# Kernel optimization log

Hardware: AMD Instinct MI355X
Metric: run time of the kernel (lower is better)

Reference implementation:

```python
import jax, jax.numpy as jnp
import numpy as np


def setup_inputs() -> dict:
    key = jax.random.key(0)
    k1, k2, k3 = jax.random.split(key, 3)
    N_GRAPHS, NUM_NODES, DEGREES = 4, 100000, 128
    BATCH = 50000
    adj_ins = jax.random.randint(k1, (N_GRAPHS, NUM_NODES, DEGREES), 0, NUM_NODES, dtype=jnp.int32)
    adj_outs = jax.random.randint(k2, (N_GRAPHS, NUM_NODES, DEGREES), 0, NUM_NODES, dtype=jnp.int32)
    ids = jax.random.randint(k3, (BATCH,), 0, NUM_NODES, dtype=jnp.int32)
    return {
        "adj_ins": adj_ins,
        "adj_outs": adj_outs,
        "g_id": 1,
        "ids": ids,
        "num_samples": 32,
        "ins": 1,
    }


def reference(adj_ins, adj_outs, g_id, ids, num_samples, ins):
    # tf.random_shuffle on the transposed [degrees, batch] matrix applies ONE
    # random permutation to the column (neighbor) axis, shared across all rows.
    adj = adj_ins if ins else adj_outs                 # [G, N, D]
    degrees = adj.shape[2]
    cur_adj_info = adj[g_id]                            # [N, D]  (slice + reshape)
    adj_lists = cur_adj_info[ids]                       # [B, D]  gather (embedding_lookup)
    perm = jax.random.permutation(jax.random.key(42), degrees)
    sel = perm[:num_samples]                            # first num_samples of shuffled cols
    return jnp.take(adj_lists, sel, axis=1)             # [B, num_samples]
```

## Files before the change

kernel.cpp:

```cpp
#include <hip/hip_runtime.h>
#include <algorithm>


static inline void tf2x32_host(unsigned k0, unsigned k1, unsigned c0, unsigned c1,
                               unsigned& o0, unsigned& o1) {
  const unsigned ks0 = k0, ks1 = k1, ks2 = k0 ^ k1 ^ 0x1BD11BDAu;
  unsigned x0 = c0 + ks0, x1 = c1 + ks1;
#define TF_R(r) { x0 += x1; x1 = (x1 << (r)) | (x1 >> (32 - (r))); x1 ^= x0; }
  TF_R(13) TF_R(15) TF_R(26) TF_R(6)   x0 += ks1; x1 += ks2 + 1u;
  TF_R(17) TF_R(29) TF_R(16) TF_R(24)  x0 += ks2; x1 += ks0 + 2u;
  TF_R(13) TF_R(15) TF_R(26) TF_R(6)   x0 += ks0; x1 += ks1 + 3u;
  TF_R(17) TF_R(29) TF_R(16) TF_R(24)  x0 += ks1; x1 += ks2 + 4u;
  TF_R(13) TF_R(15) TF_R(26) TF_R(6)   x0 += ks2; x1 += ks0 + 5u;
#undef TF_R
  o0 = x0; o1 = x1;
}

#define MAX_NS 64
struct SelArgs { int v[MAX_NS]; };

#define ROWS_PB 8
#define DEG_MAX 128
__global__ __launch_bounds__(256) void gather_rows_kernel(
    const int* __restrict__ adj_ins, const int* __restrict__ adj_outs,
    const int* __restrict__ g_id_p, const int* __restrict__ ids,
    const int* __restrict__ ins_p, const SelArgs sel,
    int batch, int ns, int num_nodes, int degrees,
    int* __restrict__ out) {
  __shared__ int s_row[ROWS_PB][DEG_MAX];
  __shared__ int s_sel[MAX_NS];

  const int t = threadIdx.x;
  const int r0 = blockIdx.x * ROWS_PB;

  if (t < ns) s_sel[t] = sel.v[t];

  const int* adj = (*ins_p) ? adj_ins : adj_outs;
  const long long base = (long long)(*g_id_p) * (long long)num_nodes * (long long)degrees;

  {
    const int row = t >> 5;
    const int lane = t & 31;
    const int r = r0 + row;
    if (r < batch) {
      const int node = ids[r];
      const int* rp = adj + base + (long long)node * degrees;
      for (int c = lane * 4; c < degrees; c += 32 * 4) {
        const int4 v = *(const int4*)(rp + c);
        *(int4*)&s_row[row][c] = v;
      }
    }
  }
  __syncthreads();

  for (int e = t; e < ROWS_PB * ns; e += 256) {
    const int row = e / ns;
    const int j = e - row * ns;
    const int r = r0 + row;
    if (r < batch) out[(long long)r * ns + j] = s_row[row][s_sel[j]];
  }
}

extern "C" void kernel_launch(void* const* d_in, const int* in_sizes, int n_in,
                              void* d_out, int out_size, void* d_ws, size_t ws_size,
                              hipStream_t stream) {
  const int* adj_ins  = (const int*)d_in[0];
  const int* adj_outs = (const int*)d_in[1];
  const int* g_id_p   = (const int*)d_in[2];
  const int* ids      = (const int*)d_in[3];
  const int* ins_p    = (const int*)d_in[5];

  const int batch = in_sizes[3];
  const int ns    = out_size / batch;
  const int NUM_NODES = 100000;
  const int DEGREES   = 128;

  unsigned sk0, sk1;
  tf2x32_host(0u, 42u, 0u, 1u, sk0, sk1);
  unsigned bits[DEG_MAX];
  int perm[DEG_MAX];
  for (int i = 0; i < DEGREES; ++i) {
    unsigned b1, b2;
    tf2x32_host(sk0, sk1, 0u, (unsigned)i, b1, b2);
    bits[i] = b1 ^ b2;
    perm[i] = i;
  }
  std::stable_sort(perm, perm + DEGREES,
                   [&](int a, int b) { return bits[a] < bits[b]; });
  SelArgs sel{};
  const int ns_c = ns > MAX_NS ? MAX_NS : ns;
  for (int j = 0; j < ns_c; ++j) sel.v[j] = perm[j];

  const int nblocks = (batch + ROWS_PB - 1) / ROWS_PB;
  gather_rows_kernel<<<nblocks, 256, 0, stream>>>(
      adj_ins, adj_outs, g_id_p, ids, ins_p, sel,
      batch, ns, NUM_NODES, DEGREES, (int*)d_out);
}
```

Measured before the change: 323.0 us.

## Replace shared-memory row staging with direct per-element gather of selected columns

Drops the staging of full adjacency rows in shared memory and the block barrier. Each thread now computes one output element and loads only the selected column straight from global memory. The aim is to avoid fetching unused columns and to remove the synchronisation, in exchange for uncoalesced scattered 4-byte loads within each row.

Result: no change. 322.7 us (-0.1%).

```diff
diff --git a/kernel.cpp b/kernel.cpp
--- a/kernel.cpp
+++ b/kernel.cpp
@@ -17,48 +17,33 @@
 }
 
 #define MAX_NS 64
+
 struct SelArgs { int v[MAX_NS]; };
 
-#define ROWS_PB 8
-#define DEG_MAX 128
-__global__ __launch_bounds__(256) void gather_rows_kernel(
+__global__ __launch_bounds__(256) void gather_direct_kernel(
     const int* __restrict__ adj_ins, const int* __restrict__ adj_outs,
     const int* __restrict__ g_id_p, const int* __restrict__ ids,
     const int* __restrict__ ins_p, const SelArgs sel,
     int batch, int ns, int num_nodes, int degrees,
     int* __restrict__ out) {
-  __shared__ int s_row[ROWS_PB][DEG_MAX];
-  __shared__ int s_sel[MAX_NS];
+  const long long gid = (long long)blockIdx.x * 256 + threadIdx.x;
 
-  const int t = threadIdx.x;
-  const int r0 = blockIdx.x * ROWS_PB;
-
-  if (t < ns) s_sel[t] = sel.v[t];
+  int r, j;
+  if (ns == 32) {
+    r = (int)(gid >> 5);
+    j = (int)(gid & 31);
+  } else {
+    r = (int)(gid / ns);
+    j = (int)(gid - (long long)r * (long long)ns);
+  }
+  if (r >= batch) return;
 
   const int* adj = (*ins_p) ? adj_ins : adj_outs;
-  const long long base = (long long)(*g_id_p) * (long long)num_nodes * (long long)degrees;
+  const long long base =
+      (long long)(*g_id_p) * (long long)num_nodes * (long long)degrees;
 
-  {
-    const int row = t >> 5;
-    const int lane = t & 31;
-    const int r = r0 + row;
-    if (r < batch) {
-      const int node = ids[r];
-      const int* rp = adj + base + (long long)node * degrees;
-      for (int c = lane * 4; c < degrees; c += 32 * 4) {
-        const int4 v = *(const int4*)(rp + c);
-        *(int4*)&s_row[row][c] = v;
-      }
-    }
-  }
-  __syncthreads();
-
-  for (int e = t; e < ROWS_PB * ns; e += 256) {
-    const int row = e / ns;
-    const int j = e - row * ns;
-    const int r = r0 + row;
-    if (r < batch) out[(long long)r * ns + j] = s_row[row][s_sel[j]];
-  }
+  const int node = ids[r];
+  out[gid] = adj[base + (long long)node * (long long)degrees + sel.v[j]];
 }
 
 extern "C" void kernel_launch(void* const* d_in, const int* in_sizes, int n_in,
@@ -77,8 +62,8 @@
 
   unsigned sk0, sk1;
   tf2x32_host(0u, 42u, 0u, 1u, sk0, sk1);
-  unsigned bits[DEG_MAX];
-  int perm[DEG_MAX];
+  unsigned bits[DEGREES];
+  int perm[DEGREES];
   for (int i = 0; i < DEGREES; ++i) {
     unsigned b1, b2;
     tf2x32_host(sk0, sk1, 0u, (unsigned)i, b1, b2);
@@ -91,8 +76,9 @@
   const int ns_c = ns > MAX_NS ? MAX_NS : ns;
   for (int j = 0; j < ns_c; ++j) sel.v[j] = perm[j];
 
-  const int nblocks = (batch + ROWS_PB - 1) / ROWS_PB;
-  gather_rows_kernel<<<nblocks, 256, 0, stream>>>(
+  const long long total = (long long)batch * (long long)ns;
+  const int nblocks = (int)((total + 255) / 256);
+  gather_direct_kernel<<<nblocks, 256, 0, stream>>>(
       adj_ins, adj_outs, g_id_p, ids, ins_p, sel,
       batch, ns, NUM_NODES, DEGREES, (int*)d_out);
 }
```
